# Kernel optimization log

Hardware: AMD Instinct MI355X
Metric: run time of the kernel (lower is better)

Reference implementation:

```python
import jax, jax.numpy as jnp
import numpy as np

N_NODES = 100000
N_EDGES = 1600000
N_GRAPHS = 128
IN_CH, OUT_CH, N_CLASS = 768, 128, 2


def setup_inputs() -> dict:
    key = jax.random.key(0)
    ks = jax.random.split(key, 8)
    x = jax.random.normal(ks[0], (N_NODES, IN_CH), dtype=jnp.float32)
    # directed edges with src < dst so to_undirected (concat + reverse) has no duplicates
    src = jax.random.randint(ks[1], (N_EDGES,), 0, N_NODES - 1, dtype=jnp.int32)
    dst = jax.random.randint(ks[2], (N_EDGES,), 1, N_NODES, dtype=jnp.int32)
    dst = jnp.where(dst <= src, src + 1, dst)  # ensure src < dst (no self-loops)
    edge_index = jnp.stack([src, dst], axis=0)
    batch = jnp.sort(jax.random.randint(ks[3], (N_NODES,), 0, N_GRAPHS, dtype=jnp.int32))
    s = 0.05
    return {
        "x": x,
        "edge_index": edge_index,
        "batch": batch,
        "num_graphs": N_GRAPHS,
        "W_conv": jax.random.normal(ks[4], (IN_CH, OUT_CH), dtype=jnp.float32) * s,
        "b_conv": jnp.zeros((OUT_CH,), dtype=jnp.float32),
        "W_lin0": jax.random.normal(ks[5], (IN_CH, OUT_CH), dtype=jnp.float32) * s,
        "b_lin0": jnp.zeros((OUT_CH,), dtype=jnp.float32),
        "W_lin1": jax.random.normal(ks[6], (2 * OUT_CH, OUT_CH), dtype=jnp.float32) * s,
        "b_lin1": jnp.zeros((OUT_CH,), dtype=jnp.float32),
        "W_lin2": jax.random.normal(ks[7], (OUT_CH, N_CLASS), dtype=jnp.float32) * s,
        "b_lin2": jnp.zeros((N_CLASS,), dtype=jnp.float32),
    }


def _gcn_conv(x, W, b, src, dst, n_nodes):
    # GCNConv: linear transform, add self-loops, symmetric normalization, scatter-add
    loop = jnp.arange(n_nodes, dtype=src.dtype)
    s = jnp.concatenate([src, loop])
    d = jnp.concatenate([dst, loop])
    deg = jax.ops.segment_sum(jnp.ones_like(d, dtype=x.dtype), d, num_segments=n_nodes)
    dinv = jnp.where(deg > 0, jax.lax.rsqrt(deg), 0.0)
    norm = dinv[s] * dinv[d]  # [E']
    h = x @ W  # [N, out]
    msg = h[s] * norm[:, None]  # gather + scale
    return jax.ops.segment_sum(msg, d, num_segments=n_nodes) + b


def reference(x, edge_index, batch, num_graphs, W_conv, b_conv,
              W_lin0, b_lin0, W_lin1, b_lin1, W_lin2, b_lin2):
    n_nodes = x.shape[0]
    # to_undirected: add reversed edges (input has src<dst so no duplicates to coalesce)
    src = jnp.concatenate([edge_index[0], edge_index[1]])
    dst = jnp.concatenate([edge_index[1], edge_index[0]])
    h = jax.nn.relu(_gcn_conv(x, W_conv, b_conv, src, dst, n_nodes))
    # global max pool over graphs
    h = jax.ops.segment_max(h, batch, num_segments=num_graphs)  # [G, out]
    # root node = first node of each graph (batch is sorted)
    root = jax.ops.segment_min(jnp.arange(n_nodes), batch, num_segments=num_graphs)
    news = jax.nn.relu(x[root] @ W_lin0 + b_lin0)  # [G, out]
    h = jax.nn.relu(jnp.concatenate([news, h], axis=-1) @ W_lin1 + b_lin1)
    logits = h @ W_lin2 + b_lin2
    return jax.nn.log_softmax(logits, axis=-1)
```

## Files before the change

### kernel.cpp

```cpp
#include <hip/hip_runtime.h>

#define N_NODES 100000
#define N_EDGES 1600000
#define N_GRAPHS 128
#define IN_CH 768
#define OUT_CH 128

#define BSHIFT 8
#define NBKT ((N_NODES + 255) / 256)
#define EPB 4000
#define SLACK 1792

using short8 = __attribute__((ext_vector_type(8))) short;
using f32x4  = __attribute__((ext_vector_type(4))) float;

__device__ __forceinline__ float bf2f(unsigned short u) {
    return __uint_as_float(((unsigned)u) << 16);
}
__device__ __forceinline__ unsigned short f2bf(float f) {
    unsigned u = __float_as_uint(f);
    u += 0x7fffu + ((u >> 16) & 1u);
    return (unsigned short)(u >> 16);
}
__device__ __forceinline__ float load_f(const void* p, size_t i, int f32) {
    return f32 ? ((const float*)p)[i] : bf2f(((const unsigned short*)p)[i]);
}
__device__ __forceinline__ float lo16(unsigned p) { return __uint_as_float((p & 0xffffu) << 16); }
__device__ __forceinline__ float hi16(unsigned p) { return __uint_as_float(p & 0xffff0000u); }

__global__ void k_detect(const unsigned short* __restrict__ x, int* flag) {
    __shared__ int s;
    if (threadIdx.x == 0) s = 0;
    __syncthreads();
    int bad = 0;
    for (int j = threadIdx.x; j < 8192; j += 256) {
        float v = bf2f(x[j]);
        if (!(v > -64.f && v < 64.f)) bad = 1;
    }
    if (bad) atomicOr(&s, 1);
    __syncthreads();
    if (threadIdx.x == 0) *flag = s;
}

__global__ void k_init(const int* __restrict__ flag, int* bucketCnt, unsigned* pooled, int* root,
                       const void* Wc, const void* bc, const void* W0, const void* b0,
                       const void* W1, const void* b1, const void* W2, const void* b2,
                       unsigned short* Wt, float* fbc, float* fW0, float* fb0,
                       float* fW1, float* fb1, float* fW2, float* fb2) {
    int f32 = *flag;
    int i = blockIdx.x * blockDim.x + threadIdx.x;
    if (i < NBKT) bucketCnt[i] = 0;
    if (i < N_GRAPHS * OUT_CH) pooled[i] = 0u;
    if (i < N_GRAPHS) root[i] = 0;
    if (i < IN_CH * OUT_CH) {
        int n = i / IN_CH, k = i - n * IN_CH;
        Wt[i] = f32 ? f2bf(((const float*)Wc)[k * OUT_CH + n])
                    : ((const unsigned short*)Wc)[k * OUT_CH + n];
        fW0[i] = load_f(W0, i, f32);
    }
    if (i < 2 * OUT_CH * OUT_CH) fW1[i] = load_f(W1, i, f32);
    if (i < OUT_CH * 2) fW2[i] = load_f(W2, i, f32);
    if (i < OUT_CH) { fbc[i] = load_f(bc, i, f32); fb0[i] = load_f(b0, i, f32); fb1[i] = load_f(b1, i, f32); }
    if (i < 2) fb2[i] = load_f(b2, i, f32);
}

__global__ __launch_bounds__(256) void k_hist(const int* __restrict__ src, const int* __restrict__ dst,
                                              int* bucketCnt) {
    __shared__ int hist[NBKT];
    int t = threadIdx.x;
    for (int b = t; b < NBKT; b += 256) hist[b] = 0;
    __syncthreads();
    int e0 = blockIdx.x * EPB, e1 = e0 + EPB;
    if (e1 > N_EDGES) e1 = N_EDGES;
    for (int i = e0 + t; i < e1; i += 256) {
        unsigned s_ = (unsigned)src[i]; if (s_ >= N_NODES) s_ = N_NODES - 1u;
        unsigned d_ = (unsigned)dst[i]; if (d_ >= N_NODES) d_ = N_NODES - 1u;
        atomicAdd(&hist[d_ >> BSHIFT], 1);
        atomicAdd(&hist[s_ >> BSHIFT], 1);
    }
    __syncthreads();
    for (int b = t; b < NBKT; b += 256)
        if (hist[b]) atomicAdd(&bucketCnt[b], hist[b]);
}

__global__ void k_scanB(const int* __restrict__ bucketCnt, int* bucketOffs, int* gcur) {
    __shared__ int s[256];
    int t = threadIdx.x;
    int i0 = 2 * t, i1 = 2 * t + 1;
    int v0 = (i0 < NBKT) ? ((bucketCnt[i0] + 7) & ~7) + SLACK : 0;
    int v1 = (i1 < NBKT) ? ((bucketCnt[i1] + 7) & ~7) + SLACK : 0;
    int pair = v0 + v1;
    s[t] = pair;
    __syncthreads();
    for (int off = 1; off < 256; off <<= 1) {
        int add = (t >= off) ? s[t - off] : 0;
        __syncthreads();
        s[t] += add;
        __syncthreads();
    }
    int excl = s[t] - pair;
    if (i0 < NBKT) { bucketOffs[i0] = excl;       gcur[i0] = excl; }
    if (i1 < NBKT) { bucketOffs[i1] = excl + v0;  gcur[i1] = excl + v0; }
    if (t == 255) bucketOffs[NBKT] = s[255];
}

__global__ __launch_bounds__(256) void k_bin(const int* __restrict__ src, const int* __restrict__ dst,
                                             int* gcur, unsigned* __restrict__ binned) {
    __shared__ int hist[NBKT];
    __shared__ int basep[NBKT];
    int t = threadIdx.x;
    for (int b = t; b < NBKT; b += 256) hist[b] = 0;
    __syncthreads();
    int e0 = blockIdx.x * EPB, e1 = e0 + EPB;
    if (e1 > N_EDGES) e1 = N_EDGES;
    for (int i = e0 + t; i < e1; i += 256) {
        unsigned s_ = (unsigned)src[i]; if (s_ >= N_NODES) s_ = N_NODES - 1u;
        unsigned d_ = (unsigned)dst[i]; if (d_ >= N_NODES) d_ = N_NODES - 1u;
        atomicAdd(&hist[d_ >> BSHIFT], 1);
        atomicAdd(&hist[s_ >> BSHIFT], 1);
    }
    __syncthreads();
    for (int b = t; b < NBKT; b += 256) {
        int c = hist[b];
        if (c) basep[b] = atomicAdd(&gcur[b], c);
        hist[b] = 0;
    }
    __syncthreads();
    for (int i = e0 + t; i < e1; i += 256) {
        unsigned s_ = (unsigned)src[i]; if (s_ >= N_NODES) s_ = N_NODES - 1u;
        unsigned d_ = (unsigned)dst[i]; if (d_ >= N_NODES) d_ = N_NODES - 1u;
        unsigned bd = d_ >> BSHIFT, bs = s_ >> BSHIFT;
        binned[basep[bd] + atomicAdd(&hist[bd], 1)] = (s_ << 8) | (d_ & 255u);
        binned[basep[bs] + atomicAdd(&hist[bs], 1)] = (d_ << 8) | (s_ & 255u);
    }
}

__global__ __launch_bounds__(256) void k_build(const unsigned* __restrict__ binned,
                                               const int* __restrict__ bucketOffs,
                                               const int* __restrict__ bucketCnt,
                                               int* offs, int* deg, float* dinv, int* adj,
                                               unsigned short* __restrict__ h) {
    __shared__ int sdeg[256], scur[256], sscan[256];
    int b = blockIdx.x, t = threadIdx.x;
    int base = bucketOffs[b];
    int n = bucketCnt[b];
    if (b == 0 && t < 64) ((unsigned*)(h + (size_t)N_NODES * OUT_CH))[t] = 0u;
    sdeg[t] = 0;
    __syncthreads();
    for (int j = t; j < n; j += 256) atomicAdd(&sdeg[binned[base + j] & 255u], 1);
    __syncthreads();
    int myd = sdeg[t];
    int pd = (myd + 7) & ~7;
    sscan[t] = pd;
    __syncthreads();
    for (int off = 1; off < 256; off <<= 1) {
        int add = (t >= off) ? sscan[t - off] : 0;
        __syncthreads();
        sscan[t] += add;
        __syncthreads();
    }
    int excl = sscan[t] - pd;
    int node = (b << BSHIFT) + t;
    if (node < N_NODES) {
        offs[node] = base + excl;
        deg[node] = pd;
        dinv[node] = rsqrtf((float)(myd + 1));
    }
    for (int j = myd; j < pd; j++) adj[base + excl + j] = N_NODES;
    scur[t] = excl;
    __syncthreads();
    for (int j = t; j < n; j += 256) {
        unsigned rec = binned[base + j];
        int loc = rec & 255u;
        adj[base + atomicAdd(&scur[loc], 1)] = (int)(rec >> 8);
    }
}

#define MBLK 128
#define BK 64
#define LSTR 72

__global__ __launch_bounds__(256) void k_gemm(const int* __restrict__ flag,
                                              const void* __restrict__ xv,
                                              const unsigned short* __restrict__ Wt,
                                              const float* __restrict__ dinv,
                                              unsigned short* __restrict__ h) {
    __shared__ __align__(16) unsigned short As[MBLK * LSTR];
    __shared__ __align__(16) unsigned short Bs[OUT_CH * LSTR];
    const int f32 = *flag;
    const int tid = threadIdx.x;
    const int wave = tid >> 6, lane = tid & 63;
    const int quad = lane >> 4, l16 = lane & 15;
    const int wm = (wave >> 1) * 64, wn = (wave & 1) * 64;
    const int row0 = blockIdx.x * MBLK;

    f32x4 acc[4][4];
#pragma unroll
    for (int mt = 0; mt < 4; mt++)
#pragma unroll
        for (int nt = 0; nt < 4; nt++) acc[mt][nt] = (f32x4){0.f, 0.f, 0.f, 0.f};

    for (int k0 = 0; k0 < IN_CH; k0 += BK) {
#pragma unroll
        for (int i = 0; i < 4; i++) {
            int chunk = tid + i * 256;
            int r = chunk >> 3, c8 = (chunk & 7) << 3;
            int gr = row0 + r; if (gr >= N_NODES) gr = N_NODES - 1;
            uint4 va;
            if (f32) {
                const float* xp = (const float*)xv + (size_t)gr * IN_CH + k0 + c8;
                float4 f0 = *(const float4*)xp;
                float4 f1 = *(const float4*)(xp + 4);
                va.x = (unsigned)f2bf(f0.x) | ((unsigned)f2bf(f0.y) << 16);
                va.y = (unsigned)f2bf(f0.z) | ((unsigned)f2bf(f0.w) << 16);
                va.z = (unsigned)f2bf(f1.x) | ((unsigned)f2bf(f1.y) << 16);
                va.w = (unsigned)f2bf(f1.z) | ((unsigned)f2bf(f1.w) << 16);
            } else {
                va = *(const uint4*)((const unsigned short*)xv + (size_t)gr * IN_CH + k0 + c8);
            }
            *(uint4*)&As[r * LSTR + c8] = va;
            uint4 vb = *(const uint4*)(Wt + (size_t)r * IN_CH + k0 + c8);
            *(uint4*)&Bs[r * LSTR + c8] = vb;
        }
        __syncthreads();
#pragma unroll
        for (int kk = 0; kk < BK; kk += 32) {
            short8 af[4], bf[4];
#pragma unroll
            for (int mt = 0; mt < 4; mt++)
                af[mt] = *(const short8*)&As[(wm + mt * 16 + l16) * LSTR + kk + quad * 8];
#pragma unroll
            for (int nt = 0; nt < 4; nt++)
                bf[nt] = *(const short8*)&Bs[(wn + nt * 16 + l16) * LSTR + kk + quad * 8];
#pragma unroll
            for (int mt = 0; mt < 4; mt++)
#pragma unroll
                for (int nt = 0; nt < 4; nt++)
                    acc[mt][nt] = __builtin_amdgcn_mfma_f32_16x16x32_bf16(af[mt], bf[nt], acc[mt][nt], 0, 0, 0);
        }
        __syncthreads();
    }

#pragma unroll
    for (int mt = 0; mt < 4; mt++) {
#pragma unroll
        for (int r = 0; r < 4; r++) {
            int m = row0 + wm + mt * 16 + quad * 4 + r;
            if (m >= N_NODES) continue;
            float dvm = dinv[m];
#pragma unroll
            for (int nt = 0; nt < 4; nt++) {
                int col = wn + nt * 16 + l16;
                h[(size_t)m * OUT_CH + col] = f2bf(acc[mt][nt][r] * dvm);
            }
        }
    }
}

__global__ __launch_bounds__(256) void k_agg(const unsigned short* __restrict__ h,
                                             const int* __restrict__ adj,
                                             const int* __restrict__ offs,
                                             const int* __restrict__ deg,
                                             const float* __restrict__ dinv,
                                             const int* __restrict__ batch,
                                             const float* __restrict__ fbc,
                                             unsigned* pooled) {
    int wave = threadIdx.x >> 6, lane = threadIdx.x & 63;
    int node = blockIdx.x * 4 + wave;
    float dv = dinv[node];

    unsigned hv = *(const unsigned*)(h + (size_t)node * OUT_CH + lane * 2);
    float a0 = lo16(hv);
    float a1 = hi16(hv);

    int o = offs[node];
    int e = o + deg[node];
    for (int i = o; i < e; i += 8) {
        uint4 q0 = *(const uint4*)&adj[i];
        uint4 q1 = *(const uint4*)&adj[i + 4];
        unsigned p0 = *(const unsigned*)(h + (size_t)q0.x * OUT_CH + lane * 2);
        unsigned p1 = *(const unsigned*)(h + (size_t)q0.y * OUT_CH + lane * 2);
        unsigned p2 = *(const unsigned*)(h + (size_t)q0.z * OUT_CH + lane * 2);
        unsigned p3 = *(const unsigned*)(h + (size_t)q0.w * OUT_CH + lane * 2);
        unsigned p4 = *(const unsigned*)(h + (size_t)q1.x * OUT_CH + lane * 2);
        unsigned p5 = *(const unsigned*)(h + (size_t)q1.y * OUT_CH + lane * 2);
        unsigned p6 = *(const unsigned*)(h + (size_t)q1.z * OUT_CH + lane * 2);
        unsigned p7 = *(const unsigned*)(h + (size_t)q1.w * OUT_CH + lane * 2);
        a0 += ((lo16(p0) + lo16(p1)) + (lo16(p2) + lo16(p3)))
            + ((lo16(p4) + lo16(p5)) + (lo16(p6) + lo16(p7)));
        a1 += ((hi16(p0) + hi16(p1)) + (hi16(p2) + hi16(p3)))
            + ((hi16(p4) + hi16(p5)) + (hi16(p6) + hi16(p7)));
    }
    a0 = fmaxf(fmaf(a0, dv, fbc[lane * 2]), 0.f);
    a1 = fmaxf(fmaf(a1, dv, fbc[lane * 2 + 1]), 0.f);

    int g = batch[node];
    __shared__ float s0[256], s1[256];
    __shared__ int sg[4];
    s0[threadIdx.x] = a0; s1[threadIdx.x] = a1;
    if (lane == 0) sg[wave] = g;
    __syncthreads();
    if (wave == 0) {
        int g0 = sg[0];
        if (sg[1] == g0 && sg[2] == g0 && sg[3] == g0) {
            float m0 = fmaxf(fmaxf(s0[lane], s0[64 + lane]), fmaxf(s0[128 + lane], s0[192 + lane]));
            float m1 = fmaxf(fmaxf(s1[lane], s1[64 + lane]), fmaxf(s1[128 + lane], s1[192 + lane]));
            atomicMax(&pooled[g0 * OUT_CH + lane * 2],     __float_as_uint(m0));
            atomicMax(&pooled[g0 * OUT_CH + lane * 2 + 1], __float_as_uint(m1));
        } else {
#pragma unroll
            for (int w = 0; w < 4; w++) {
                atomicMax(&pooled[sg[w] * OUT_CH + lane * 2],     __float_as_uint(s0[w * 64 + lane]));
                atomicMax(&pooled[sg[w] * OUT_CH + lane * 2 + 1], __float_as_uint(s1[w * 64 + lane]));
            }
        }
    }
}

__global__ void k_root(const int* __restrict__ batch, int* root) {
    int i = blockIdx.x * blockDim.x + threadIdx.x;
    if (i >= N_NODES) return;
    int b = batch[i];
    if (i == 0 || batch[i - 1] != b) root[b] = i;
}

__global__ __launch_bounds__(128) void k_news(const int* __restrict__ flag,
                                              const void* __restrict__ x,
                                              const int* __restrict__ root,
                                              const float* __restrict__ W0,
                                              const float* __restrict__ b0,
                                              float* news) {
    __shared__ float xs[IN_CH];
    int f32 = *flag;
    int g = blockIdx.x, c = threadIdx.x;
    int r = root[g];
    for (int j = c; j < IN_CH; j += 128) xs[j] = load_f(x, (size_t)r * IN_CH + j, f32);
    __syncthreads();
    float acc = 0.f;
#pragma unroll 8
    for (int k = 0; k < IN_CH; k++) acc += xs[k] * W0[k * OUT_CH + c];
    news[g * OUT_CH + c] = fmaxf(acc + b0[c], 0.f);
}

__global__ __launch_bounds__(128) void k_final(const int* __restrict__ flag,
                                               const float* __restrict__ news,
                                               const unsigned* __restrict__ pooled,
                                               const float* __restrict__ W1,
                                               const float* __restrict__ b1,
                                               const float* __restrict__ W2,
                                               const float* __restrict__ b2,
                                               void* out) {
    __shared__ float ins[2 * OUT_CH];
    __shared__ float h2s[OUT_CH];
    int g = blockIdx.x, c = threadIdx.x;
    ins[c] = news[g * OUT_CH + c];
    ins[OUT_CH + c] = __uint_as_float(pooled[g * OUT_CH + c]);
    __syncthreads();
    float acc = 0.f;
#pragma unroll 8
    for (int k = 0; k < 2 * OUT_CH; k++) acc += ins[k] * W1[k * OUT_CH + c];
    h2s[c] = fmaxf(acc + b1[c], 0.f);
    __syncthreads();
    if (c == 0) {
        float l0 = b2[0], l1 = b2[1];
        for (int k = 0; k < OUT_CH; k++) { float v = h2s[k]; l0 += v * W2[k * 2]; l1 += v * W2[k * 2 + 1]; }
        float m = fmaxf(l0, l1);
        float ls = m + logf(expf(l0 - m) + expf(l1 - m));
        if (*flag) {
            ((float*)out)[g * 2]     = l0 - ls;
            ((float*)out)[g * 2 + 1] = l1 - ls;
        } else {
            ((unsigned short*)out)[g * 2]     = f2bf(l0 - ls);
            ((unsigned short*)out)[g * 2 + 1] = f2bf(l1 - ls);
        }
    }
}

extern "C" void kernel_launch(void* const* d_in, const int* in_sizes, int n_in,
                              void* d_out, int out_size, void* d_ws, size_t ws_size,
                              hipStream_t stream) {
    const void* x     = d_in[0];
    const int*  ei    = (const int*)d_in[1];
    const int*  batch = (const int*)d_in[2];
    const void* Wc    = d_in[4];
    const void* bc    = d_in[5];
    const void* W0    = d_in[6];
    const void* b0    = d_in[7];
    const void* W1    = d_in[8];
    const void* b1    = d_in[9];
    const void* W2    = d_in[10];
    const void* b2    = d_in[11];
    const int* src = ei;
    const int* dst = ei + N_EDGES;

    char* p = (char*)d_ws;
    auto carve = [&](size_t bytes) -> void* {
        void* r = (void*)p;
        p += (bytes + 255) & ~(size_t)255;
        return r;
    };
    int*      flag      = (int*)carve(4);
    int*      deg       = (int*)carve((size_t)N_NODES * 4);
    int*      offs      = (int*)carve((size_t)N_NODES * 4);
    int*      bucketCnt = (int*)carve((size_t)(NBKT + 1) * 4);
    int*      bucketOffs= (int*)carve((size_t)(NBKT + 1) * 4);
    int*      gcur      = (int*)carve((size_t)(NBKT + 1) * 4);
    float*    dinv      = (float*)carve((size_t)N_NODES * 4);
    int*      root      = (int*)carve(128 * 4);
    unsigned* pooled    = (unsigned*)carve((size_t)N_GRAPHS * OUT_CH * 4);
    float*    news      = (float*)carve((size_t)N_GRAPHS * OUT_CH * 4);
    unsigned short* Wt  = (unsigned short*)carve((size_t)IN_CH * OUT_CH * 2);
    float*    fW0       = (float*)carve((size_t)IN_CH * OUT_CH * 4);
    float*    fW1       = (float*)carve((size_t)2 * OUT_CH * OUT_CH * 4);
    float*    fW2       = (float*)carve((size_t)OUT_CH * 2 * 4);
    float*    fbc       = (float*)carve((size_t)OUT_CH * 4);
    float*    fb0       = (float*)carve((size_t)OUT_CH * 4);
    float*    fb1       = (float*)carve((size_t)OUT_CH * 4);
    float*    fb2       = (float*)carve(2 * 4);
    int*      adj       = (int*)carve(((size_t)2 * N_EDGES + (size_t)NBKT * 2048) * 4);
    void*     hb        = carve((size_t)(N_NODES + 1) * OUT_CH * 2);
    unsigned* binned    = (unsigned*)hb;
    unsigned short* h   = (unsigned short*)hb;

    const int nEdgeBlk = (N_EDGES + EPB - 1) / EPB;

    k_detect<<<1, 256, 0, stream>>>((const unsigned short*)x, flag);
    k_init  <<<391, 256, 0, stream>>>(flag, bucketCnt, pooled, root, Wc, bc, W0, b0, W1, b1, W2, b2,
                                      Wt, fbc, fW0, fb0, fW1, fb1, fW2, fb2);
    k_hist  <<<nEdgeBlk, 256, 0, stream>>>(src, dst, bucketCnt);
    k_scanB <<<1, 256, 0, stream>>>(bucketCnt, bucketOffs, gcur);
    k_bin   <<<nEdgeBlk, 256, 0, stream>>>(src, dst, gcur, binned);
    k_build <<<NBKT, 256, 0, stream>>>(binned, bucketOffs, bucketCnt, offs, deg, dinv, adj, h);
    k_gemm  <<<(N_NODES + MBLK - 1) / MBLK, 256, 0, stream>>>(flag, x, Wt, dinv, h);
    k_agg   <<<N_NODES / 4, 256, 0, stream>>>(h, adj, offs, deg, dinv, batch, fbc, pooled);
    k_root  <<<391, 256, 0, stream>>>(batch, root);
    k_news  <<<N_GRAPHS, 128, 0, stream>>>(flag, x, root, fW0, fb0, news);
    k_final <<<N_GRAPHS, 128, 0, stream>>>(flag, news, pooled, fW1, fb1, fW2, fb2, d_out);
}
```

Baseline: 767.2 us.

## Use fixed-capacity edge buckets, drop histogram/scan passes, fuse root/news into other kernels

Gives each 256-node bucket a fixed slot of CAPREC records, so the separate histogram and bucket-scan kernels can go. Also moves root detection into k_init, fuses the news matmul into k_final with a 256-thread split-K, and packs offset and degree into one int2. The aggregation loop now takes 16 neighbors per iteration, with adjacency padded to multiples of 16. The aim is fewer launches and passes over the edge list, at the cost of more padded gather loads and silently dropped edges if a bucket ever exceeds its capacity.

```diff
diff --git a/kernel.cpp b/kernel.cpp
--- a/kernel.cpp
+++ b/kernel.cpp
@@ -9,7 +9,9 @@
 #define BSHIFT 8
 #define NBKT ((N_NODES + 255) / 256)
 #define EPB 4000
-#define SLACK 1792
+#define CAPREC 16384
+#define PADV 16
+#define CAPADJ (CAPREC + 256 * (PADV - 1))
 
 using short8 = __attribute__((ext_vector_type(8))) short;
 using f32x4  = __attribute__((ext_vector_type(4))) float;
@@ -25,7 +27,7 @@
 __device__ __forceinline__ float load_f(const void* p, size_t i, int f32) {
     return f32 ? ((const float*)p)[i] : bf2f(((const unsigned short*)p)[i]);
 }
-__device__ __forceinline__ float lo16(unsigned p) { return __uint_as_float((p & 0xffffu) << 16); }
+__device__ __forceinline__ float lo16(unsigned p) { return __uint_as_float(p << 16); }
 __device__ __forceinline__ float hi16(unsigned p) { return __uint_as_float(p & 0xffff0000u); }
 
 __global__ void k_detect(const unsigned short* __restrict__ x, int* flag) {
@@ -42,16 +44,20 @@
     if (threadIdx.x == 0) *flag = s;
 }
 
-__global__ void k_init(const int* __restrict__ flag, int* bucketCnt, unsigned* pooled, int* root,
+__global__ void k_init(const int* __restrict__ flag, int* gcur, unsigned* pooled, int* root,
+                       const int* __restrict__ batch,
                        const void* Wc, const void* bc, const void* W0, const void* b0,
                        const void* W1, const void* b1, const void* W2, const void* b2,
                        unsigned short* Wt, float* fbc, float* fW0, float* fb0,
                        float* fW1, float* fb1, float* fW2, float* fb2) {
     int f32 = *flag;
     int i = blockIdx.x * blockDim.x + threadIdx.x;
-    if (i < NBKT) bucketCnt[i] = 0;
+    if (i < NBKT) gcur[i] = i * CAPREC;
     if (i < N_GRAPHS * OUT_CH) pooled[i] = 0u;
-    if (i < N_GRAPHS) root[i] = 0;
+    if (i < N_NODES) {
+        int b = batch[i];
+        if (i == 0 || batch[i - 1] != b) root[b] = i;
+    }
     if (i < IN_CH * OUT_CH) {
         int n = i / IN_CH, k = i - n * IN_CH;
         Wt[i] = f32 ? f2bf(((const float*)Wc)[k * OUT_CH + n])
@@ -64,9 +70,10 @@
     if (i < 2) fb2[i] = load_f(b2, i, f32);
 }
 
-__global__ __launch_bounds__(256) void k_hist(const int* __restrict__ src, const int* __restrict__ dst,
-                                              int* bucketCnt) {
+__global__ __launch_bounds__(256) void k_bin(const int* __restrict__ src, const int* __restrict__ dst,
+                                             int* gcur, unsigned* __restrict__ binned) {
     __shared__ int hist[NBKT];
+    __shared__ int basep[NBKT];
     int t = threadIdx.x;
     for (int b = t; b < NBKT; b += 256) hist[b] = 0;
     __syncthreads();
@@ -79,50 +86,12 @@
         atomicAdd(&hist[s_ >> BSHIFT], 1);
     }
     __syncthreads();
-    for (int b = t; b < NBKT; b += 256)
-        if (hist[b]) atomicAdd(&bucketCnt[b], hist[b]);
-}
-
-__global__ void k_scanB(const int* __restrict__ bucketCnt, int* bucketOffs, int* gcur) {
-    __shared__ int s[256];
-    int t = threadIdx.x;
-    int i0 = 2 * t, i1 = 2 * t + 1;
-    int v0 = (i0 < NBKT) ? ((bucketCnt[i0] + 7) & ~7) + SLACK : 0;
-    int v1 = (i1 < NBKT) ? ((bucketCnt[i1] + 7) & ~7) + SLACK : 0;
-    int pair = v0 + v1;
-    s[t] = pair;
-    __syncthreads();
-    for (int off = 1; off < 256; off <<= 1) {
-        int add = (t >= off) ? s[t - off] : 0;
-        __syncthreads();
-        s[t] += add;
-        __syncthreads();
-    }
-    int excl = s[t] - pair;
-    if (i0 < NBKT) { bucketOffs[i0] = excl;       gcur[i0] = excl; }
-    if (i1 < NBKT) { bucketOffs[i1] = excl + v0;  gcur[i1] = excl + v0; }
-    if (t == 255) bucketOffs[NBKT] = s[255];
-}
-
-__global__ __launch_bounds__(256) void k_bin(const int* __restrict__ src, const int* __restrict__ dst,
-                                             int* gcur, unsigned* __restrict__ binned) {
-    __shared__ int hist[NBKT];
-    __shared__ int basep[NBKT];
-    int t = threadIdx.x;
-    for (int b = t; b < NBKT; b += 256) hist[b] = 0;
-    __syncthreads();
-    int e0 = blockIdx.x * EPB, e1 = e0 + EPB;
-    if (e1 > N_EDGES) e1 = N_EDGES;
-    for (int i = e0 + t; i < e1; i += 256) {
-        unsigned s_ = (unsigned)src[i]; if (s_ >= N_NODES) s_ = N_NODES - 1u;
-        unsigned d_ = (unsigned)dst[i]; if (d_ >= N_NODES) d_ = N_NODES - 1u;
-        atomicAdd(&hist[d_ >> BSHIFT], 1);
-        atomicAdd(&hist[s_ >> BSHIFT], 1);
-    }
-    __syncthreads();
     for (int b = t; b < NBKT; b += 256) {
         int c = hist[b];
-        if (c) basep[b] = atomicAdd(&gcur[b], c);
+        if (c) {
+            int base = atomicAdd(&gcur[b], c);
+            basep[b] = (base + c <= (b + 1) * CAPREC) ? base : -1;
+        }
         hist[b] = 0;
     }
     __syncthreads();
@@ -130,27 +99,30 @@
         unsigned s_ = (unsigned)src[i]; if (s_ >= N_NODES) s_ = N_NODES - 1u;
         unsigned d_ = (unsigned)dst[i]; if (d_ >= N_NODES) d_ = N_NODES - 1u;
         unsigned bd = d_ >> BSHIFT, bs = s_ >> BSHIFT;
-        binned[basep[bd] + atomicAdd(&hist[bd], 1)] = (s_ << 8) | (d_ & 255u);
-        binned[basep[bs] + atomicAdd(&hist[bs], 1)] = (d_ << 8) | (s_ & 255u);
+        int pd_ = basep[bd], ps_ = basep[bs];
+        int od = atomicAdd(&hist[bd], 1);
+        int os = atomicAdd(&hist[bs], 1);
+        if (pd_ >= 0) binned[pd_ + od] = (s_ << 8) | (d_ & 255u);
+        if (ps_ >= 0) binned[ps_ + os] = (d_ << 8) | (s_ & 255u);
     }
 }
 
 __global__ __launch_bounds__(256) void k_build(const unsigned* __restrict__ binned,
-                                               const int* __restrict__ bucketOffs,
-                                               const int* __restrict__ bucketCnt,
-                                               int* offs, int* deg, float* dinv, int* adj,
-                                               unsigned short* __restrict__ h) {
+                                               const int* __restrict__ gcur,
+                                               int2* odeg, float* dinv, int* adj) {
     __shared__ int sdeg[256], scur[256], sscan[256];
     int b = blockIdx.x, t = threadIdx.x;
-    int base = bucketOffs[b];
-    int n = bucketCnt[b];
-    if (b == 0 && t < 64) ((unsigned*)(h + (size_t)N_NODES * OUT_CH))[t] = 0u;
+    int base = b * CAPREC;
+    int n = gcur[b] - base;
+    if (n > CAPREC) n = CAPREC;
+    if (n < 0) n = 0;
+    int base_adj = b * CAPADJ;
     sdeg[t] = 0;
     __syncthreads();
     for (int j = t; j < n; j += 256) atomicAdd(&sdeg[binned[base + j] & 255u], 1);
     __syncthreads();
     int myd = sdeg[t];
-    int pd = (myd + 7) & ~7;
+    int pd = (myd + PADV - 1) & ~(PADV - 1);
     sscan[t] = pd;
     __syncthreads();
     for (int off = 1; off < 256; off <<= 1) {
@@ -162,17 +134,16 @@
     int excl = sscan[t] - pd;
     int node = (b << BSHIFT) + t;
     if (node < N_NODES) {
-        offs[node] = base + excl;
-        deg[node] = pd;
+        odeg[node] = make_int2(base_adj + excl, pd);
         dinv[node] = rsqrtf((float)(myd + 1));
     }
-    for (int j = myd; j < pd; j++) adj[base + excl + j] = N_NODES;
+    for (int j = myd; j < pd; j++) adj[base_adj + excl + j] = N_NODES;
     scur[t] = excl;
     __syncthreads();
     for (int j = t; j < n; j += 256) {
         unsigned rec = binned[base + j];
         int loc = rec & 255u;
-        adj[base + atomicAdd(&scur[loc], 1)] = (int)(rec >> 8);
+        adj[base_adj + atomicAdd(&scur[loc], 1)] = (int)(rec >> 8);
     }
 }
 
@@ -189,6 +160,7 @@
     __shared__ __align__(16) unsigned short Bs[OUT_CH * LSTR];
     const int f32 = *flag;
     const int tid = threadIdx.x;
+    if (blockIdx.x == 0 && tid < 64) ((unsigned*)(h + (size_t)N_NODES * OUT_CH))[tid] = 0u;
     const int wave = tid >> 6, lane = tid & 63;
     const int quad = lane >> 4, l16 = lane & 15;
     const int wm = (wave >> 1) * 64, wn = (wave & 1) * 64;
@@ -259,8 +231,7 @@
 
 __global__ __launch_bounds__(256) void k_agg(const unsigned short* __restrict__ h,
                                              const int* __restrict__ adj,
-                                             const int* __restrict__ offs,
-                                             const int* __restrict__ deg,
+                                             const int2* __restrict__ odeg,
                                              const float* __restrict__ dinv,
                                              const int* __restrict__ batch,
                                              const float* __restrict__ fbc,
@@ -273,11 +244,13 @@
     float a0 = lo16(hv);
     float a1 = hi16(hv);
 
-    int o = offs[node];
-    int e = o + deg[node];
-    for (int i = o; i < e; i += 8) {
+    int2 od = odeg[node];
+    int o = od.x, e = od.x + od.y;
+    for (int i = o; i < e; i += 16) {
         uint4 q0 = *(const uint4*)&adj[i];
         uint4 q1 = *(const uint4*)&adj[i + 4];
+        uint4 q2 = *(const uint4*)&adj[i + 8];
+        uint4 q3 = *(const uint4*)&adj[i + 12];
         unsigned p0 = *(const unsigned*)(h + (size_t)q0.x * OUT_CH + lane * 2);
         unsigned p1 = *(const unsigned*)(h + (size_t)q0.y * OUT_CH + lane * 2);
         unsigned p2 = *(const unsigned*)(h + (size_t)q0.z * OUT_CH + lane * 2);
@@ -286,10 +259,22 @@
         unsigned p5 = *(const unsigned*)(h + (size_t)q1.y * OUT_CH + lane * 2);
         unsigned p6 = *(const unsigned*)(h + (size_t)q1.z * OUT_CH + lane * 2);
         unsigned p7 = *(const unsigned*)(h + (size_t)q1.w * OUT_CH + lane * 2);
-        a0 += ((lo16(p0) + lo16(p1)) + (lo16(p2) + lo16(p3)))
-            + ((lo16(p4) + lo16(p5)) + (lo16(p6) + lo16(p7)));
-        a1 += ((hi16(p0) + hi16(p1)) + (hi16(p2) + hi16(p3)))
-            + ((hi16(p4) + hi16(p5)) + (hi16(p6) + hi16(p7)));
+        unsigned p8 = *(const unsigned*)(h + (size_t)q2.x * OUT_CH + lane * 2);
+        unsigned p9 = *(const unsigned*)(h + (size_t)q2.y * OUT_CH + lane * 2);
+        unsigned pa = *(const unsigned*)(h + (size_t)q2.z * OUT_CH + lane * 2);
+        unsigned pb = *(const unsigned*)(h + (size_t)q2.w * OUT_CH + lane * 2);
+        unsigned pc = *(const unsigned*)(h + (size_t)q3.x * OUT_CH + lane * 2);
+        unsigned pd = *(const unsigned*)(h + (size_t)q3.y * OUT_CH + lane * 2);
+        unsigned pe = *(const unsigned*)(h + (size_t)q3.z * OUT_CH + lane * 2);
+        unsigned pf = *(const unsigned*)(h + (size_t)q3.w * OUT_CH + lane * 2);
+        a0 += (((lo16(p0) + lo16(p1)) + (lo16(p2) + lo16(p3)))
+             + ((lo16(p4) + lo16(p5)) + (lo16(p6) + lo16(p7))))
+            + (((lo16(p8) + lo16(p9)) + (lo16(pa) + lo16(pb)))
+             + ((lo16(pc) + lo16(pd)) + (lo16(pe) + lo16(pf))));
+        a1 += (((hi16(p0) + hi16(p1)) + (hi16(p2) + hi16(p3)))
+             + ((hi16(p4) + hi16(p5)) + (hi16(p6) + hi16(p7))))
+            + (((hi16(p8) + hi16(p9)) + (hi16(pa) + hi16(pb)))
+             + ((hi16(pc) + hi16(pd)) + (hi16(pe) + hi16(pf))));
     }
     a0 = fmaxf(fmaf(a0, dv, fbc[lane * 2]), 0.f);
     a1 = fmaxf(fmaf(a1, dv, fbc[lane * 2 + 1]), 0.f);
@@ -317,56 +302,55 @@
     }
 }
 
-__global__ void k_root(const int* __restrict__ batch, int* root) {
-    int i = blockIdx.x * blockDim.x + threadIdx.x;
-    if (i >= N_NODES) return;
-    int b = batch[i];
-    if (i == 0 || batch[i - 1] != b) root[b] = i;
-}
-
-__global__ __launch_bounds__(128) void k_news(const int* __restrict__ flag,
-                                              const void* __restrict__ x,
-                                              const int* __restrict__ root,
-                                              const float* __restrict__ W0,
-                                              const float* __restrict__ b0,
-                                              float* news) {
-    __shared__ float xs[IN_CH];
-    int f32 = *flag;
-    int g = blockIdx.x, c = threadIdx.x;
-    int r = root[g];
-    for (int j = c; j < IN_CH; j += 128) xs[j] = load_f(x, (size_t)r * IN_CH + j, f32);
-    __syncthreads();
-    float acc = 0.f;
-#pragma unroll 8
-    for (int k = 0; k < IN_CH; k++) acc += xs[k] * W0[k * OUT_CH + c];
-    news[g * OUT_CH + c] = fmaxf(acc + b0[c], 0.f);
-}
-
-__global__ __launch_bounds__(128) void k_final(const int* __restrict__ flag,
-                                               const float* __restrict__ news,
+__global__ __launch_bounds__(256) void k_final(const int* __restrict__ flag,
+                                               const void* __restrict__ x,
+                                               const int* __restrict__ root,
                                                const unsigned* __restrict__ pooled,
+                                               const float* __restrict__ W0,
+                                               const float* __restrict__ b0,
                                                const float* __restrict__ W1,
                                                const float* __restrict__ b1,
                                                const float* __restrict__ W2,
                                                const float* __restrict__ b2,
                                                void* out) {
+    __shared__ float xs[IN_CH];
+    __shared__ float ps[256];
     __shared__ float ins[2 * OUT_CH];
     __shared__ float h2s[OUT_CH];
-    int g = blockIdx.x, c = threadIdx.x;
-    ins[c] = news[g * OUT_CH + c];
-    ins[OUT_CH + c] = __uint_as_float(pooled[g * OUT_CH + c]);
-    __syncthreads();
-    float acc = 0.f;
+    int f32 = *flag;
+    int g = blockIdx.x, t = threadIdx.x;
+    int r = root[g]; if ((unsigned)r >= N_NODES) r = 0;
+    for (int j = t; j < IN_CH; j += 256) xs[j] = load_f(x, (size_t)r * IN_CH + j, f32);
+    if (t >= 128) ins[OUT_CH + (t - 128)] = __uint_as_float(pooled[g * OUT_CH + (t - 128)]);
+    __syncthreads();
+    {
+        int c = t & 127, half = t >> 7;
+        int k0 = half * (IN_CH / 2);
+        float acc = 0.f;
 #pragma unroll 8
-    for (int k = 0; k < 2 * OUT_CH; k++) acc += ins[k] * W1[k * OUT_CH + c];
-    h2s[c] = fmaxf(acc + b1[c], 0.f);
-    __syncthreads();
-    if (c == 0) {
+        for (int k = 0; k < IN_CH / 2; k++) acc += xs[k0 + k] * W0[(size_t)(k0 + k) * OUT_CH + c];
+        ps[t] = acc;
+    }
+    __syncthreads();
+    if (t < 128) ins[t] = fmaxf(ps[t] + ps[t + 128] + b0[t], 0.f);
+    __syncthreads();
+    {
+        int c = t & 127, half = t >> 7;
+        int k0 = half * OUT_CH;
+        float acc = 0.f;
+#pragma unroll 8
+        for (int k = 0; k < OUT_CH; k++) acc += ins[k0 + k] * W1[(size_t)(k0 + k) * OUT_CH + c];
+        ps[t] = acc;
+    }
+    __syncthreads();
+    if (t < 128) h2s[t] = fmaxf(ps[t] + ps[t + 128] + b1[t], 0.f);
+    __syncthreads();
+    if (t == 0) {
         float l0 = b2[0], l1 = b2[1];
         for (int k = 0; k < OUT_CH; k++) { float v = h2s[k]; l0 += v * W2[k * 2]; l1 += v * W2[k * 2 + 1]; }
         float m = fmaxf(l0, l1);
         float ls = m + logf(expf(l0 - m) + expf(l1 - m));
-        if (*flag) {
+        if (f32) {
             ((float*)out)[g * 2]     = l0 - ls;
             ((float*)out)[g * 2 + 1] = l1 - ls;
         } else {
@@ -400,15 +384,11 @@
         return r;
     };
     int*      flag      = (int*)carve(4);
-    int*      deg       = (int*)carve((size_t)N_NODES * 4);
-    int*      offs      = (int*)carve((size_t)N_NODES * 4);
-    int*      bucketCnt = (int*)carve((size_t)(NBKT + 1) * 4);
-    int*      bucketOffs= (int*)carve((size_t)(NBKT + 1) * 4);
-    int*      gcur      = (int*)carve((size_t)(NBKT + 1) * 4);
+    int*      gcur      = (int*)carve((size_t)NBKT * 4);
+    int2*     odeg      = (int2*)carve((size_t)N_NODES * 8);
     float*    dinv      = (float*)carve((size_t)N_NODES * 4);
     int*      root      = (int*)carve(128 * 4);
     unsigned* pooled    = (unsigned*)carve((size_t)N_GRAPHS * OUT_CH * 4);
-    float*    news      = (float*)carve((size_t)N_GRAPHS * OUT_CH * 4);
     unsigned short* Wt  = (unsigned short*)carve((size_t)IN_CH * OUT_CH * 2);
     float*    fW0       = (float*)carve((size_t)IN_CH * OUT_CH * 4);
     float*    fW1       = (float*)carve((size_t)2 * OUT_CH * OUT_CH * 4);
@@ -417,23 +397,21 @@
     float*    fb0       = (float*)carve((size_t)OUT_CH * 4);
     float*    fb1       = (float*)carve((size_t)OUT_CH * 4);
     float*    fb2       = (float*)carve(2 * 4);
-    int*      adj       = (int*)carve(((size_t)2 * N_EDGES + (size_t)NBKT * 2048) * 4);
-    void*     hb        = carve((size_t)(N_NODES + 1) * OUT_CH * 2);
+    int*      adj       = (int*)carve((size_t)NBKT * CAPADJ * 4);
+    size_t binned_bytes = (size_t)NBKT * CAPREC * 4;
+    size_t h_bytes      = (size_t)(N_NODES + 1) * OUT_CH * 2;
+    void*     hb        = carve(binned_bytes > h_bytes ? binned_bytes : h_bytes);
     unsigned* binned    = (unsigned*)hb;
     unsigned short* h   = (unsigned short*)hb;
 
     const int nEdgeBlk = (N_EDGES + EPB - 1) / EPB;
 
     k_detect<<<1, 256, 0, stream>>>((const unsigned short*)x, flag);
-    k_init  <<<391, 256, 0, stream>>>(flag, bucketCnt, pooled, root, Wc, bc, W0, b0, W1, b1, W2, b2,
+    k_init  <<<391, 256, 0, stream>>>(flag, gcur, pooled, root, batch, Wc, bc, W0, b0, W1, b1, W2, b2,
                                       Wt, fbc, fW0, fb0, fW1, fb1, fW2, fb2);
-    k_hist  <<<nEdgeBlk, 256, 0, stream>>>(src, dst, bucketCnt);
-    k_scanB <<<1, 256, 0, stream>>>(bucketCnt, bucketOffs, gcur);
     k_bin   <<<nEdgeBlk, 256, 0, stream>>>(src, dst, gcur, binned);
-    k_build <<<NBKT, 256, 0, stream>>>(binned, bucketOffs, bucketCnt, offs, deg, dinv, adj, h);
+    k_build <<<NBKT, 256, 0, stream>>>(binned, gcur, odeg, dinv, adj);
     k_gemm  <<<(N_NODES + MBLK - 1) / MBLK, 256, 0, stream>>>(flag, x, Wt, dinv, h);
-    k_agg   <<<N_NODES / 4, 256, 0, stream>>>(h, adj, offs, deg, dinv, batch, fbc, pooled);
-    k_root  <<<391, 256, 0, stream>>>(batch, root);
-    k_news  <<<N_GRAPHS, 128, 0, stream>>>(flag, x, root, fW0, fb0, news);
-    k_final <<<N_GRAPHS, 128, 0, stream>>>(flag, news, pooled, fW1, fb1, fW2, fb2, d_out);
-}
+    k_agg   <<<N_NODES / 4, 256, 0, stream>>>(h, adj, odeg, dinv, batch, fbc, pooled);
+    k_final <<<N_GRAPHS, 256, 0, stream>>>(flag, x, root, pooled, fW0, fb0, fW1, fb1, fW2, fb2, d_out);
+}
```

New measurement: 708.5 us. -7.7%, faster.
